# Kernel tuning notes

Measured on AMD Instinct MI355X. Metric: run time of the kernel, lower is better.

Reference implementation:

```python
import jax, jax.numpy as jnp
import numpy as np

B = 4194304  # batch of 3x3 rotation matrices


def _make_rotations(key, b):
    k1, k2 = jax.random.split(key)
    axis = jax.random.normal(k1, (b, 3), dtype=jnp.float32)
    axis = axis / jnp.linalg.norm(axis, axis=1, keepdims=True)
    # angles bounded away from 0 and pi (s_theta = 2*sin(theta) must be nonzero)
    theta = jax.random.uniform(k2, (b,), dtype=jnp.float32, minval=0.1, maxval=np.pi - 0.1)
    x, y, z = axis[:, 0], axis[:, 1], axis[:, 2]
    zero = jnp.zeros_like(x)
    K = jnp.stack([zero, -z, y, z, zero, -x, -y, x, zero], axis=1).reshape(b, 3, 3)
    I = jnp.eye(3, dtype=jnp.float32)
    s = jnp.sin(theta)[:, None, None]
    c = jnp.cos(theta)[:, None, None]
    return I + s * K + (1.0 - c) * (K @ K)  # Rodrigues


def setup_inputs() -> dict:
    key = jax.random.key(0)
    return {"mat_batch": _make_rotations(key, B)}


def reference(mat_batch) -> jnp.ndarray:
    # rotation angle from trace: theta = acos((tr(R) - 1) / 2)
    tr = jnp.trace(mat_batch, axis1=1, axis2=2)  # [B]
    rot_angle = jnp.arccos((tr - 1.0) / 2.0)[:, None]  # [B,1]
    s_theta = 2.0 * jnp.sin(rot_angle)  # [B,1]
    # unnormalized axis from skew-symmetric part
    w = jnp.stack(
        [
            mat_batch[:, 2, 1] - mat_batch[:, 1, 2],
            mat_batch[:, 0, 2] - mat_batch[:, 2, 0],
            mat_batch[:, 1, 0] - mat_batch[:, 0, 1],
        ],
        axis=1,
    )  # [B,3]
    rot_axis = w / s_theta
    return rot_angle * rot_axis  # [B,3] twist = theta * axis
```

## Files before the change

### kernel.cpp

```cpp
#include <hip/hip_runtime.h>
#include <math.h>


__global__ __launch_bounds__(256) void mat2twist_lds_kernel(
    const float4* __restrict__ in4,
    float4* __restrict__ out4,
    int n_quads,
    const float* __restrict__ in_s,
    float* __restrict__ out_s,
    int n_mat) {

    __shared__ float4 lds[256 * 9];

    const int t = threadIdx.x;

    for (int qbase = blockIdx.x * 256; qbase < n_quads; qbase += gridDim.x * 256) {
        const int quads_here = min(256, n_quads - qbase);
        const int in_total4  = quads_here * 9;

        const float4* src = in4 + (size_t)qbase * 9;
        for (int i = t; i < in_total4; i += 256) {
            lds[i] = src[i];
        }
        __syncthreads();

        float r[12];
        const bool active = t < quads_here;
        if (active) {
            const float* m = (const float*)(lds + t * 9);
#pragma unroll
            for (int j = 0; j < 4; ++j) {
                const float* a = m + 9 * j;
                float tr  = a[0] + a[4] + a[8];
                float c   = 0.5f * (tr - 1.0f);
                float ang = acosf(c);
                float s2  = fmaxf(1.0f - c * c, 1e-30f);
                float k   = ang * 0.5f / sqrtf(s2);
                r[3 * j + 0] = k * (a[7] - a[5]);
                r[3 * j + 1] = k * (a[2] - a[6]);
                r[3 * j + 2] = k * (a[3] - a[1]);
            }
        }
        __syncthreads();

        if (active) {
            lds[t * 3 + 0] = make_float4(r[0], r[1], r[2],  r[3]);
            lds[t * 3 + 1] = make_float4(r[4], r[5], r[6],  r[7]);
            lds[t * 3 + 2] = make_float4(r[8], r[9], r[10], r[11]);
        }
        __syncthreads();

        float4* dst = out4 + (size_t)qbase * 3;
        const int out_total4 = quads_here * 3;
        for (int i = t; i < out_total4; i += 256) {
            dst[i] = lds[i];
        }
        __syncthreads();
    }

    if (blockIdx.x == 0 && t == 0) {
        for (int i = n_quads * 4; i < n_mat; ++i) {
            const float* a = in_s + (size_t)i * 9;
            float tr  = a[0] + a[4] + a[8];
            float c   = 0.5f * (tr - 1.0f);
            float ang = acosf(c);
            float s2  = fmaxf(1.0f - c * c, 1e-30f);
            float k   = ang * 0.5f / sqrtf(s2);
            out_s[3 * i + 0] = k * (a[7] - a[5]);
            out_s[3 * i + 1] = k * (a[2] - a[6]);
            out_s[3 * i + 2] = k * (a[3] - a[1]);
        }
    }
}

extern "C" void kernel_launch(void* const* d_in, const int* in_sizes, int n_in,
                              void* d_out, int out_size, void* d_ws, size_t ws_size,
                              hipStream_t stream) {
    const float* in = (const float*)d_in[0];
    float* out = (float*)d_out;
    const int n_mat   = in_sizes[0] / 9;
    const int n_quads = n_mat / 4;

    int grid = (n_quads + 255) / 256;
    if (grid > 8192) grid = 8192;
    if (grid < 1) grid = 1;

    mat2twist_lds_kernel<<<grid, 256, 0, stream>>>(
        (const float4*)in, (float4*)out, n_quads, in, out, n_mat);
}
```

Measured before the change: 225.5 us.

## Split into full-block main kernel and tail kernel, write output directly

Replaces the grid-stride loop with one block per 1024 matrices, loading nine float4 per thread up front with no bounds checks, then storing results straight to global memory instead of staging them through LDS. Leftover matrices go to a separate tail kernel instead of a single serial thread. It also swaps the divide by sqrt for rsqrtf. This cuts barriers and LDS traffic and exposes more loads in flight, at the cost of uncoalesced strided float4 output stores and a larger grid of short-lived blocks.

```diff
diff --git a/kernel.cpp b/kernel.cpp
--- a/kernel.cpp
+++ b/kernel.cpp
@@ -2,74 +2,58 @@
 #include <math.h>
 
 
-__global__ __launch_bounds__(256) void mat2twist_lds_kernel(
+__device__ __forceinline__ void twist1(const float* __restrict__ a,
+                                       float* __restrict__ r) {
+    float tr  = a[0] + a[4] + a[8];
+    float c   = 0.5f * (tr - 1.0f);
+    float ang = acosf(c);
+    float s2  = fmaxf(1.0f - c * c, 1e-30f);
+    float k   = ang * 0.5f * rsqrtf(s2);
+    r[0] = k * (a[7] - a[5]);
+    r[1] = k * (a[2] - a[6]);
+    r[2] = k * (a[3] - a[1]);
+}
+
+__global__ __launch_bounds__(256) void mat2twist_main(
     const float4* __restrict__ in4,
-    float4* __restrict__ out4,
-    int n_quads,
-    const float* __restrict__ in_s,
-    float* __restrict__ out_s,
-    int n_mat) {
+    float4* __restrict__ out4) {
 
     __shared__ float4 lds[256 * 9];
+    const int t = threadIdx.x;
+    const size_t qb = (size_t)blockIdx.x * 256;
 
-    const int t = threadIdx.x;
+    const float4* __restrict__ src = in4 + qb * 9;
+    float4 v[9];
+#pragma unroll
+    for (int j = 0; j < 9; ++j) v[j] = src[t + 256 * j];
+#pragma unroll
+    for (int j = 0; j < 9; ++j) lds[t + 256 * j] = v[j];
+    __syncthreads();
 
-    for (int qbase = blockIdx.x * 256; qbase < n_quads; qbase += gridDim.x * 256) {
-        const int quads_here = min(256, n_quads - qbase);
-        const int in_total4  = quads_here * 9;
+    const float* m = (const float*)(lds + (size_t)t * 9);
+    float r[12];
+#pragma unroll
+    for (int j = 0; j < 4; ++j) twist1(m + 9 * j, r + 3 * j);
 
-        const float4* src = in4 + (size_t)qbase * 9;
-        for (int i = t; i < in_total4; i += 256) {
-            lds[i] = src[i];
-        }
-        __syncthreads();
+    float4* __restrict__ dst = out4 + qb * 3 + (size_t)t * 3;
+    dst[0] = make_float4(r[0], r[1], r[2],  r[3]);
+    dst[1] = make_float4(r[4], r[5], r[6],  r[7]);
+    dst[2] = make_float4(r[8], r[9], r[10], r[11]);
+}
 
-        float r[12];
-        const bool active = t < quads_here;
-        if (active) {
-            const float* m = (const float*)(lds + t * 9);
+__global__ __launch_bounds__(256) void mat2twist_tail(
+    const float* __restrict__ in, float* __restrict__ out,
+    int start, int n_mat) {
+    int i = start + blockIdx.x * blockDim.x + threadIdx.x;
+    if (i < n_mat) {
+        float a[9];
 #pragma unroll
-            for (int j = 0; j < 4; ++j) {
-                const float* a = m + 9 * j;
-                float tr  = a[0] + a[4] + a[8];
-                float c   = 0.5f * (tr - 1.0f);
-                float ang = acosf(c);
-                float s2  = fmaxf(1.0f - c * c, 1e-30f);
-                float k   = ang * 0.5f / sqrtf(s2);
-                r[3 * j + 0] = k * (a[7] - a[5]);
-                r[3 * j + 1] = k * (a[2] - a[6]);
-                r[3 * j + 2] = k * (a[3] - a[1]);
-            }
-        }
-        __syncthreads();
-
-        if (active) {
-            lds[t * 3 + 0] = make_float4(r[0], r[1], r[2],  r[3]);
-            lds[t * 3 + 1] = make_float4(r[4], r[5], r[6],  r[7]);
-            lds[t * 3 + 2] = make_float4(r[8], r[9], r[10], r[11]);
-        }
-        __syncthreads();
-
-        float4* dst = out4 + (size_t)qbase * 3;
-        const int out_total4 = quads_here * 3;
-        for (int i = t; i < out_total4; i += 256) {
-            dst[i] = lds[i];
-        }
-        __syncthreads();
-    }
-
-    if (blockIdx.x == 0 && t == 0) {
-        for (int i = n_quads * 4; i < n_mat; ++i) {
-            const float* a = in_s + (size_t)i * 9;
-            float tr  = a[0] + a[4] + a[8];
-            float c   = 0.5f * (tr - 1.0f);
-            float ang = acosf(c);
-            float s2  = fmaxf(1.0f - c * c, 1e-30f);
-            float k   = ang * 0.5f / sqrtf(s2);
-            out_s[3 * i + 0] = k * (a[7] - a[5]);
-            out_s[3 * i + 1] = k * (a[2] - a[6]);
-            out_s[3 * i + 2] = k * (a[3] - a[1]);
-        }
+        for (int j = 0; j < 9; ++j) a[j] = in[(size_t)i * 9 + j];
+        float r[3];
+        twist1(a, r);
+        out[(size_t)i * 3 + 0] = r[0];
+        out[(size_t)i * 3 + 1] = r[1];
+        out[(size_t)i * 3 + 2] = r[2];
     }
 }
 
@@ -78,13 +62,17 @@
                               hipStream_t stream) {
     const float* in = (const float*)d_in[0];
     float* out = (float*)d_out;
-    const int n_mat   = in_sizes[0] / 9;
-    const int n_quads = n_mat / 4;
+    const int n_mat = in_sizes[0] / 9;
 
-    int grid = (n_quads + 255) / 256;
-    if (grid > 8192) grid = 8192;
-    if (grid < 1) grid = 1;
-
-    mat2twist_lds_kernel<<<grid, 256, 0, stream>>>(
-        (const float4*)in, (float4*)out, n_quads, in, out, n_mat);
+    const int full_blocks = n_mat / 1024;
+    if (full_blocks > 0) {
+        mat2twist_main<<<full_blocks, 256, 0, stream>>>(
+            (const float4*)in, (float4*)out);
+    }
+    const int start = full_blocks * 1024;
+    const int rem = n_mat - start;
+    if (rem > 0) {
+        mat2twist_tail<<<(rem + 255) / 256, 256, 0, stream>>>(
+            in, out, start, n_mat);
+    }
 }
```

Result: no change. 221.9 us (-1.6%).
